# Performance work log

Measured on AMD Instinct MI355X. Metric: run time of the kernel, lower is better.

Reference implementation:

```python
import jax, jax.numpy as jnp
import numpy as np

H = 512  # hidden_size


def setup_inputs() -> dict:
    key = jax.random.key(0)
    ks = jax.random.split(key, 8)
    B, L = 16, 2048
    query = jax.random.normal(ks[0], (B, 1, 2 * H), dtype=jnp.float32)
    keys = jax.random.normal(ks[1], (B, L, 2 * H), dtype=jnp.float32)
    coverage = jax.random.uniform(ks[2], (B, L, 1), dtype=jnp.float32)
    # alignment MLP: Linear(4H+1 -> 2H, bias) -> tanh -> Linear(2H -> 1, no bias) -> softmax(dim=1)
    s1 = 1.0 / np.sqrt(4 * H + 1)
    W1 = jax.random.uniform(ks[3], (4 * H + 1, 2 * H), jnp.float32, -s1, s1)
    b1 = jax.random.uniform(ks[4], (2 * H,), jnp.float32, -s1, s1)
    s2 = 1.0 / np.sqrt(2 * H)
    W2 = jax.random.uniform(ks[5], (2 * H, 1), jnp.float32, -s2, s2)
    # reduce: Linear(2H -> H, no bias)
    Wr = jax.random.uniform(ks[6], (2 * H, H), jnp.float32, -s2, s2)
    return {"query": query, "keys": keys, "coverage": coverage,
            "W1": W1, "b1": b1, "W2": W2, "Wr": Wr}


def reference(query, keys, coverage, W1, b1, W2, Wr):
    B, L, _ = keys.shape
    q = jnp.broadcast_to(query, (B, L, query.shape[-1]))          # (B,L,2H)
    feat = jnp.concatenate([q, keys, coverage], axis=-1)          # (B,L,4H+1)
    h = jnp.tanh(feat @ W1 + b1)                                  # (B,L,2H)
    scores = h @ W2                                               # (B,L,1)
    attention = jax.nn.softmax(scores, axis=1)                    # softmax over length
    reduced = keys @ Wr                                           # (B,L,H)
    context = jnp.einsum('blo,blh->boh', attention, reduced)      # (B,1,H)
    return context, attention
```

## Files before the change

kernel.cpp:

```cpp
#include <hip/hip_runtime.h>
#include <hip/hip_bf16.h>
#include <stdint.h>

typedef short bf16x8 __attribute__((ext_vector_type(8)));
typedef float f32x4 __attribute__((ext_vector_type(4)));
typedef unsigned int u32x2 __attribute__((ext_vector_type(2)));

__device__ __forceinline__ uint32_t pack2f(float lo, float hi) {
  union { __hip_bfloat162 h; uint32_t u; } c;
  c.h.x = __float2bfloat16(lo);
  c.h.y = __float2bfloat16(hi);
  return c.u;
}

__device__ __forceinline__ unsigned short f32_to_bf16(float f) {
  union { __hip_bfloat16 h; unsigned short u; } c;
  c.h = __float2bfloat16(f);
  return c.u;
}

__device__ __forceinline__ float bfbits_to_f32(uint32_t hi16) {
  union { uint32_t u; float f; } c;
  c.u = hi16 << 16;
  return c.f;
}

__device__ __forceinline__ float fast_tanh(float x) {
  float e = __builtin_amdgcn_exp2f(x * 2.8853900817779268f);
  return 1.0f - 2.0f * __builtin_amdgcn_rcpf(e + 1.0f);
}

#define GLD16(g, l)                                                                    \
  __builtin_amdgcn_global_load_lds((const __attribute__((address_space(1))) void*)(g), \
                                   (__attribute__((address_space(3))) void*)(l), 16, 0, 0)

#define MFMA16(a, b, c) __builtin_amdgcn_mfma_f32_16x16x32_bf16(a, b, c, 0, 0, 0)
#define SBAR0() __builtin_amdgcn_sched_barrier(0)

__global__ void prep_kernel(const float* __restrict__ keys, unsigned short* __restrict__ keysbf,
                            const float* __restrict__ W1, unsigned short* __restrict__ W1kt,
                            const float* __restrict__ query, const float* __restrict__ b1,
                            float* __restrict__ qterm) {
  __shared__ __align__(16) unsigned char smem[16896];
  const int bid = blockIdx.x;
  const int t = threadIdx.x;
  if (bid < 256) {
    float (*tt)[65] = (float(*)[65])smem;
    const int kb = (bid & 15) * 64;
    const int jb = (bid >> 4) * 64;
    const int c = t & 63;
    const int r = t >> 6;
#pragma unroll
    for (int i = 0; i < 16; ++i) {
      const int k = i * 4 + r;
      tt[k][c] = W1[(size_t)(1024 + kb + k) * 1024 + (jb + c)];
    }
    __syncthreads();
#pragma unroll
    for (int i = 0; i < 16; ++i) {
      const int j = i * 4 + r;
      W1kt[(size_t)(jb + j) * 1024 + (kb + c)] = f32_to_bf16(tt[c][j]);
    }
  } else if (bid < 512) {
    float (*part)[64] = (float(*)[64])smem;
    const int q = bid - 256;
    const int b = q >> 4;
    const int j = (q & 15) * 64 + (t & 63);
    const int kq = t >> 6;
    const float* qp = query + b * 1024 + kq * 256;
    const float* wp = W1 + (size_t)(kq * 256) * 1024 + j;
    float acc = 0.f;
#pragma unroll 8
    for (int k = 0; k < 256; ++k) acc += qp[k] * wp[(size_t)k * 1024];
    part[kq][t & 63] = acc;
    __syncthreads();
    if (t < 64) {
      const int jj = (q & 15) * 64 + t;
      qterm[b * 1024 + jj] = b1[jj] + part[0][t] + part[1][t] + part[2][t] + part[3][t];
    }
  } else {
    const size_t base = (size_t)(bid - 512) * 16384;
#pragma unroll
    for (int bt = 0; bt < 2; ++bt) {
      f32x4 v[8];
#pragma unroll
      for (int i = 0; i < 8; ++i)
        v[i] = *(const f32x4*)(keys + base + bt * 8192 + i * 1024 + t * 4);
#pragma unroll
      for (int i = 0; i < 8; ++i) {
        u32x2 p;
        p.x = pack2f(v[i].x, v[i].y);
        p.y = pack2f(v[i].z, v[i].w);
        *(u32x2*)(keysbf + base + bt * 8192 + i * 1024 + t * 4) = p;
      }
    }
  }
}


#define V16_STAGE(kt_, P)                                            \
  GLD16(gkA + (kt_) * 64 + 0 * 65536, (P) + 0 * 8192 + t16);         \
  GLD16(gwB + (kt_) * 64 + 0 * 65536, (P) + 32768 + 0 * 8192 + t16); \
  GLD16(gkA + (kt_) * 64 + 1 * 65536, (P) + 1 * 8192 + t16);         \
  GLD16(gwB + (kt_) * 64 + 1 * 65536, (P) + 32768 + 1 * 8192 + t16); \
  GLD16(gkA + (kt_) * 64 + 2 * 65536, (P) + 2 * 8192 + t16);         \
  GLD16(gwB + (kt_) * 64 + 2 * 65536, (P) + 32768 + 2 * 8192 + t16); \
  GLD16(gkA + (kt_) * 64 + 3 * 65536, (P) + 3 * 8192 + t16);         \
  GLD16(gwB + (kt_) * 64 + 3 * 65536, (P) + 32768 + 3 * 8192 + t16);

#define V16_COMPUTE(P)                                                           \
  _Pragma("unroll") for (int kk = 0; kk < 2; ++kk) {                             \
    bf16x8 af[8], bfv[4];                                                        \
    _Pragma("unroll") for (int mf = 0; mf < 8; ++mf)                             \
        af[mf] = *(const bf16x8*)((P) + ((abase + mf * 2048) ^ (kk * 64)));      \
    _Pragma("unroll") for (int nf = 0; nf < 4; ++nf)                             \
        bfv[nf] = *(const bf16x8*)((P) + ((bbase + nf * 2048) ^ (kk * 64)));     \
    __builtin_amdgcn_s_setprio(1);                                               \
    _Pragma("unroll") for (int nf = 0; nf < 4; ++nf)                             \
        _Pragma("unroll") for (int mf = 0; mf < 8; ++mf) acc[mf][nf] =           \
            MFMA16(af[mf], bfv[nf], acc[mf][nf]);                                \
    __builtin_amdgcn_s_setprio(0);                                               \
  }

#define V16_ITER(t_, Pc, Ps, LAST)                            \
  asm volatile("s_waitcnt vmcnt(0) lgkmcnt(0)" ::: "memory"); \
  __builtin_amdgcn_s_barrier();                               \
  SBAR0();                                                    \
  if (!(LAST)) { V16_STAGE((t_) + 1, Ps); }                   \
  SBAR0();                                                    \
  V16_COMPUTE(Pc);

#define V16_PAIR(t0, t1)      \
  V16_ITER(t0, P0, P1, false) \
  V16_ITER(t1, P1, P0, (t1) == 15)

__global__ __launch_bounds__(512, 2) void gemm_score_v16(
    const unsigned short* __restrict__ keysbf, const unsigned short* __restrict__ W1kt,
    const float* __restrict__ qterm, const float* __restrict__ coverage,
    const float* __restrict__ W1, const float* __restrict__ W2,
    float* __restrict__ scores_part) {
  __shared__ __align__(16) unsigned char lds[135168];
  unsigned char* P0 = lds;
  unsigned char* P1 = lds + 65536;
  float* Sred = (float*)(lds + 131072);

  const int tid = threadIdx.x;
  const int bid = blockIdx.x;
  const int xcd = bid & 7;
  const int idx = bid >> 3;
  const int rowt = xcd * 16 + (idx >> 2);
  const int colgrp = idx & 3;
  const int row0 = rowt * 256;
  const int col0 = colgrp * 256;
  const int b = row0 >> 11;
  const int w = tid >> 6;
  const int wm = w >> 2, wn = w & 3;
  const int lane = tid & 63;
  const int c16 = lane & 15, q4 = lane >> 4;

  const int swzc = (q4 ^ (c16 & 7)) << 4;
  const int abase = (wm * 128 + c16) * 128 + swzc;
  const int bbase = 32768 + (wn * 64 + c16) * 128 + swzc;

  const int sr = tid >> 3;
  const int su = (tid & 7) ^ (sr & 7);
  const unsigned short* gkA = keysbf + (size_t)(row0 + sr) * 1024 + su * 8;
  const unsigned short* gwB = W1kt + (size_t)(col0 + sr) * 1024 + su * 8;
  const int t16 = tid * 16;

  f32x4 acc[8][4];
  const f32x4 zz = {0.f, 0.f, 0.f, 0.f};
#pragma unroll
  for (int mf = 0; mf < 8; ++mf)
#pragma unroll
    for (int nf = 0; nf < 4; ++nf) acc[mf][nf] = zz;

  V16_STAGE(0, P0);

  V16_PAIR(0, 1)
  V16_PAIR(2, 3)
  V16_PAIR(4, 5)
  V16_PAIR(6, 7)
  V16_PAIR(8, 9)
  V16_PAIR(10, 11)
  V16_PAIR(12, 13)
  V16_PAIR(14, 15)

  float covv[8][4];
#pragma unroll
  for (int mf = 0; mf < 8; ++mf)
#pragma unroll
    for (int r = 0; r < 4; ++r)
      covv[mf][r] = coverage[row0 + wm * 128 + mf * 16 + q4 * 4 + r];

  float p_part[8][4];
#pragma unroll
  for (int mf = 0; mf < 8; ++mf)
#pragma unroll
    for (int r = 0; r < 4; ++r) p_part[mf][r] = 0.f;

#pragma unroll
  for (int nf = 0; nf < 4; ++nf) {
    const int col = col0 + wn * 64 + nf * 16 + c16;
    const float qt = qterm[b * 1024 + col];
    const float w1c = W1[(size_t)2048 * 1024 + col];
    const float w2 = W2[col];
#pragma unroll
    for (int mf = 0; mf < 8; ++mf)
#pragma unroll
      for (int r = 0; r < 4; ++r) {
        float v = acc[mf][nf][r] + qt + covv[mf][r] * w1c;
        p_part[mf][r] += fast_tanh(v) * w2;
      }
  }

#pragma unroll
  for (int mf = 0; mf < 8; ++mf)
#pragma unroll
    for (int r = 0; r < 4; ++r) {
      float p = p_part[mf][r];
      p += __shfl_xor(p, 1);
      p += __shfl_xor(p, 2);
      p += __shfl_xor(p, 4);
      p += __shfl_xor(p, 8);
      if (c16 == 0) Sred[w * 128 + mf * 16 + q4 * 4 + r] = p;
    }
  __syncthreads();
  if (tid < 256) {
    const int wmv = tid >> 7, rl = tid & 127;
    float s = Sred[(wmv * 4 + 0) * 128 + rl] + Sred[(wmv * 4 + 1) * 128 + rl] +
              Sred[(wmv * 4 + 2) * 128 + rl] + Sred[(wmv * 4 + 3) * 128 + rl];
    scores_part[(size_t)colgrp * 32768 + row0 + tid] = s;
  }
}

__global__ void ctxpre_fused(const unsigned short* __restrict__ keysbf,
                             const float* __restrict__ sp, float* __restrict__ att,
                             float* __restrict__ ctx_part) {
  __shared__ float sc[2048];
  __shared__ float red[4];
  __shared__ float att_s[128];
  const int b = blockIdx.x;
  const int sl = blockIdx.y;
  const int tid = threadIdx.x;
  float mx = -1e30f;
  for (int l = tid; l < 2048; l += 256) {
    float v = 0.f;
#pragma unroll
    for (int g = 0; g < 4; ++g) v += sp[(size_t)g * 32768 + b * 2048 + l];
    sc[l] = v;
    mx = fmaxf(mx, v);
  }
#pragma unroll
  for (int o = 1; o < 64; o <<= 1) mx = fmaxf(mx, __shfl_xor(mx, o));
  if ((tid & 63) == 0) red[tid >> 6] = mx;
  __syncthreads();
  mx = fmaxf(fmaxf(red[0], red[1]), fmaxf(red[2], red[3]));
  __syncthreads();
  float sum = 0.f;
  for (int l = tid; l < 2048; l += 256) sum += __expf(sc[l] - mx);
#pragma unroll
  for (int o = 1; o < 64; o <<= 1) sum += __shfl_xor(sum, o);
  if ((tid & 63) == 0) red[tid >> 6] = sum;
  __syncthreads();
  const float inv = 1.0f / (red[0] + red[1] + red[2] + red[3]);
  if (tid < 128) {
    const float a = __expf(sc[sl * 128 + tid] - mx) * inv;
    att_s[tid] = a;
    att[b * 2048 + sl * 128 + tid] = a;
  }
  __syncthreads();

  const unsigned short* kb = keysbf + ((size_t)b * 2048 + sl * 128) * 1024 + tid * 4;
  f32x4 acc = {0.f, 0.f, 0.f, 0.f};
#pragma unroll 4
  for (int l = 0; l < 128; ++l) {
    u32x2 v = *(const u32x2*)(kb + (size_t)l * 1024);
    const float al = att_s[l];
    acc.x += bfbits_to_f32(v.x & 0xFFFFu) * al;
    acc.y += bfbits_to_f32(v.x >> 16) * al;
    acc.z += bfbits_to_f32(v.y & 0xFFFFu) * al;
    acc.w += bfbits_to_f32(v.y >> 16) * al;
  }
  *(f32x4*)(ctx_part + ((size_t)(sl * 16 + b)) * 1024 + tid * 4) = acc;
}

__global__ void ctx2_kernel(const float* __restrict__ ctx_part, const float* __restrict__ Wr,
                            float* __restrict__ out) {
  __shared__ float cpre[1024];
  __shared__ float part[4][64];
  const int hb = blockIdx.x;
  const int b = blockIdx.y;
  const int t = threadIdx.x;
#pragma unroll
  for (int jj = 0; jj < 4; ++jj) {
    const int j = jj * 256 + t;
    float s = 0.f;
#pragma unroll
    for (int sl = 0; sl < 16; ++sl) s += ctx_part[((size_t)(sl * 16 + b)) * 1024 + j];
    cpre[j] = s;
  }
  __syncthreads();
  const int h = hb * 64 + (t & 63);
  const int jq = t >> 6;
  const float* wp = Wr + (size_t)(jq * 256) * 512 + h;
  float acc = 0.f;
#pragma unroll 8
  for (int k = 0; k < 256; ++k) acc += cpre[jq * 256 + k] * wp[(size_t)k * 512];
  part[jq][t & 63] = acc;
  __syncthreads();
  if (t < 64)
    out[b * 512 + hb * 64 + t] = part[0][t] + part[1][t] + part[2][t] + part[3][t];
}

extern "C" void kernel_launch(void* const* d_in, const int* in_sizes, int n_in, void* d_out,
                              int out_size, void* d_ws, size_t ws_size, hipStream_t stream) {
  const float* query = (const float*)d_in[0];
  const float* keys = (const float*)d_in[1];
  const float* coverage = (const float*)d_in[2];
  const float* W1 = (const float*)d_in[3];
  const float* b1 = (const float*)d_in[4];
  const float* W2 = (const float*)d_in[5];
  const float* Wr = (const float*)d_in[6];
  float* out = (float*)d_out;
  char* ws = (char*)d_ws;

  float* scores_part = (float*)ws;
  float* ctx_part = (float*)(ws + 524288);
  float* qterm = (float*)(ws + 1638400);
  unsigned short* W1kt = (unsigned short*)(ws + 1703936);
  unsigned short* keysbf = (unsigned short*)(ws + 3801088);

  float* context_out = out;
  float* att_out = out + 8192;

  prep_kernel<<<dim3(2560), dim3(256), 0, stream>>>(keys, keysbf, W1, W1kt, query, b1, qterm);
  gemm_score_v16<<<dim3(512), dim3(512), 0, stream>>>(keysbf, W1kt, qterm, coverage, W1, W2,
                                                      scores_part);
  ctxpre_fused<<<dim3(16, 16), dim3(256), 0, stream>>>(keysbf, scores_part, att_out, ctx_part);
  ctx2_kernel<<<dim3(8, 16), dim3(256), 0, stream>>>(ctx_part, Wr, context_out);
}
```

Measured before the change: 131.4 us.

## Fuse keys fp32-to-bf16 conversion into GEMM A-operand load path

Removes the keys conversion blocks from the prep kernel. The GEMM now loads fp32 keys directly into registers, converts them to bf16, and writes them into swizzled LDS, prefetching two tiles ahead and waiting only on partial vmcnt. Blocks in column group 0 also write the bf16 keys to global memory for the later context kernel. This avoids a separate full pass over keys, but each of the four column groups re-reads fp32 keys, the staging goes through registers, and launch bounds drop to one block per CU.

```diff
diff --git a/kernel.cpp b/kernel.cpp
--- a/kernel.cpp
+++ b/kernel.cpp
@@ -37,10 +37,9 @@
 #define MFMA16(a, b, c) __builtin_amdgcn_mfma_f32_16x16x32_bf16(a, b, c, 0, 0, 0)
 #define SBAR0() __builtin_amdgcn_sched_barrier(0)
 
-__global__ void prep_kernel(const float* __restrict__ keys, unsigned short* __restrict__ keysbf,
-                            const float* __restrict__ W1, unsigned short* __restrict__ W1kt,
-                            const float* __restrict__ query, const float* __restrict__ b1,
-                            float* __restrict__ qterm) {
+__global__ void prep2_kernel(const float* __restrict__ W1, unsigned short* __restrict__ W1kt,
+                             const float* __restrict__ query, const float* __restrict__ b1,
+                             float* __restrict__ qterm) {
   __shared__ __align__(16) unsigned char smem[16896];
   const int bid = blockIdx.x;
   const int t = threadIdx.x;
@@ -61,7 +60,7 @@
       const int j = i * 4 + r;
       W1kt[(size_t)(jb + j) * 1024 + (kb + c)] = f32_to_bf16(tt[c][j]);
     }
-  } else if (bid < 512) {
+  } else {
     float (*part)[64] = (float(*)[64])smem;
     const int q = bid - 256;
     const int b = q >> 4;
@@ -78,37 +77,35 @@
       const int jj = (q & 15) * 64 + t;
       qterm[b * 1024 + jj] = b1[jj] + part[0][t] + part[1][t] + part[2][t] + part[3][t];
     }
-  } else {
-    const size_t base = (size_t)(bid - 512) * 16384;
-#pragma unroll
-    for (int bt = 0; bt < 2; ++bt) {
-      f32x4 v[8];
-#pragma unroll
-      for (int i = 0; i < 8; ++i)
-        v[i] = *(const f32x4*)(keys + base + bt * 8192 + i * 1024 + t * 4);
-#pragma unroll
-      for (int i = 0; i < 8; ++i) {
-        u32x2 p;
-        p.x = pack2f(v[i].x, v[i].y);
-        p.y = pack2f(v[i].z, v[i].w);
-        *(u32x2*)(keysbf + base + bt * 8192 + i * 1024 + t * 4) = p;
-      }
-    }
-  }
-}
-
-
-#define V16_STAGE(kt_, P)                                            \
-  GLD16(gkA + (kt_) * 64 + 0 * 65536, (P) + 0 * 8192 + t16);         \
+  }
+}
+
+
+#define V17_LOAD_A(kt_)                                \
+  _Pragma("unroll") for (int i = 0; i < 8; ++i)        \
+      Ar[i] = *(const f32x4*)(gkeys + (size_t)i * 32768 + (kt_) * 64);
+
+#define V17_PACK()                                     \
+  _Pragma("unroll") for (int i = 0; i < 8; ++i) {      \
+    pk[i].x = pack2f(Ar[i].x, Ar[i].y);                \
+    pk[i].y = pack2f(Ar[i].z, Ar[i].w);                \
+  }
+
+#define V17_WRITE_A(Ps)                                \
+  _Pragma("unroll") for (int i = 0; i < 8; ++i)        \
+      *(u32x2*)((Ps) + awof + i * 4096) = pk[i];
+
+#define V17_STORE(kt_)                                 \
+  _Pragma("unroll") for (int i = 0; i < 8; ++i)        \
+      *(u32x2*)(gkbf + (size_t)i * 32768 + (kt_) * 64) = pk[i];
+
+#define V17_STAGE_B(kt_, P)                                          \
   GLD16(gwB + (kt_) * 64 + 0 * 65536, (P) + 32768 + 0 * 8192 + t16); \
-  GLD16(gkA + (kt_) * 64 + 1 * 65536, (P) + 1 * 8192 + t16);         \
   GLD16(gwB + (kt_) * 64 + 1 * 65536, (P) + 32768 + 1 * 8192 + t16); \
-  GLD16(gkA + (kt_) * 64 + 2 * 65536, (P) + 2 * 8192 + t16);         \
   GLD16(gwB + (kt_) * 64 + 2 * 65536, (P) + 32768 + 2 * 8192 + t16); \
-  GLD16(gkA + (kt_) * 64 + 3 * 65536, (P) + 3 * 8192 + t16);         \
   GLD16(gwB + (kt_) * 64 + 3 * 65536, (P) + 32768 + 3 * 8192 + t16);
 
-#define V16_COMPUTE(P)                                                           \
+#define V17_COMPUTE(P)                                                           \
   _Pragma("unroll") for (int kk = 0; kk < 2; ++kk) {                             \
     bf16x8 af[8], bfv[4];                                                        \
     _Pragma("unroll") for (int mf = 0; mf < 8; ++mf)                             \
@@ -122,23 +119,32 @@
     __builtin_amdgcn_s_setprio(0);                                               \
   }
 
-#define V16_ITER(t_, Pc, Ps, LAST)                            \
-  asm volatile("s_waitcnt vmcnt(0) lgkmcnt(0)" ::: "memory"); \
-  __builtin_amdgcn_s_barrier();                               \
-  SBAR0();                                                    \
-  if (!(LAST)) { V16_STAGE((t_) + 1, Ps); }                   \
-  SBAR0();                                                    \
-  V16_COMPUTE(Pc);
-
-#define V16_PAIR(t0, t1)      \
-  V16_ITER(t0, P0, P1, false) \
-  V16_ITER(t1, P1, P0, (t1) == 15)
-
-__global__ __launch_bounds__(512, 2) void gemm_score_v16(
-    const unsigned short* __restrict__ keysbf, const unsigned short* __restrict__ W1kt,
-    const float* __restrict__ qterm, const float* __restrict__ coverage,
-    const float* __restrict__ W1, const float* __restrict__ W2,
-    float* __restrict__ scores_part) {
+#define V17_ITER(t_, Pc, Ps, LAST)                                       \
+  if (LAST) { asm volatile("s_waitcnt vmcnt(0) lgkmcnt(0)" ::: "memory"); } \
+  else      { asm volatile("s_waitcnt vmcnt(8) lgkmcnt(0)" ::: "memory"); } \
+  __builtin_amdgcn_s_barrier();                                          \
+  SBAR0();                                                               \
+  if (!(LAST)) {                                                         \
+    V17_PACK();                                                          \
+    V17_WRITE_A(Ps);                                                     \
+    if (cg0) { V17_STORE((t_) + 1); }                                    \
+    SBAR0();                                                             \
+    V17_STAGE_B((t_) + 1, Ps);                                           \
+    SBAR0();                                                             \
+    if ((t_) < 14) { V17_LOAD_A((t_) + 2); }                             \
+    SBAR0();                                                             \
+  }                                                                      \
+  V17_COMPUTE(Pc);
+
+#define V17_PAIR(t0, t1)      \
+  V17_ITER(t0, P0, P1, false) \
+  V17_ITER(t1, P1, P0, (t1) == 15)
+
+__global__ __launch_bounds__(512, 1) void gemm_score_v17(
+    const float* __restrict__ keys, unsigned short* __restrict__ keysbf,
+    const unsigned short* __restrict__ W1kt, const float* __restrict__ qterm,
+    const float* __restrict__ coverage, const float* __restrict__ W1,
+    const float* __restrict__ W2, float* __restrict__ scores_part) {
   __shared__ __align__(16) unsigned char lds[135168];
   unsigned char* P0 = lds;
   unsigned char* P1 = lds + 65536;
@@ -150,6 +156,7 @@
   const int idx = bid >> 3;
   const int rowt = xcd * 16 + (idx >> 2);
   const int colgrp = idx & 3;
+  const bool cg0 = (colgrp == 0);
   const int row0 = rowt * 256;
   const int col0 = colgrp * 256;
   const int b = row0 >> 11;
@@ -162,12 +169,19 @@
   const int abase = (wm * 128 + c16) * 128 + swzc;
   const int bbase = 32768 + (wn * 64 + c16) * 128 + swzc;
 
+  const int ar0 = tid >> 4;
+  const int kun = tid & 15;
+  const float* gkeys = keys + (size_t)(row0 + ar0) * 1024 + kun * 4;
+  unsigned short* gkbf = keysbf + (size_t)(row0 + ar0) * 1024 + kun * 4;
+  const int awof = ar0 * 128 + ((((kun >> 1) ^ (ar0 & 7)) << 4) + (kun & 1) * 8);
+
   const int sr = tid >> 3;
   const int su = (tid & 7) ^ (sr & 7);
-  const unsigned short* gkA = keysbf + (size_t)(row0 + sr) * 1024 + su * 8;
   const unsigned short* gwB = W1kt + (size_t)(col0 + sr) * 1024 + su * 8;
   const int t16 = tid * 16;
 
+  f32x4 Ar[8];
+  u32x2 pk[8];
   f32x4 acc[8][4];
   const f32x4 zz = {0.f, 0.f, 0.f, 0.f};
 #pragma unroll
@@ -175,16 +189,24 @@
 #pragma unroll
     for (int nf = 0; nf < 4; ++nf) acc[mf][nf] = zz;
 
-  V16_STAGE(0, P0);
-
-  V16_PAIR(0, 1)
-  V16_PAIR(2, 3)
-  V16_PAIR(4, 5)
-  V16_PAIR(6, 7)
-  V16_PAIR(8, 9)
-  V16_PAIR(10, 11)
-  V16_PAIR(12, 13)
-  V16_PAIR(14, 15)
+  V17_LOAD_A(0);
+  V17_PACK();
+  V17_WRITE_A(P0);
+  if (cg0) { V17_STORE(0); }
+  SBAR0();
+  V17_STAGE_B(0, P0);
+  SBAR0();
+  V17_LOAD_A(1);
+  SBAR0();
+
+  V17_PAIR(0, 1)
+  V17_PAIR(2, 3)
+  V17_PAIR(4, 5)
+  V17_PAIR(6, 7)
+  V17_PAIR(8, 9)
+  V17_PAIR(10, 11)
+  V17_PAIR(12, 13)
+  V17_PAIR(14, 15)
 
   float covv[8][4];
 #pragma unroll
@@ -334,9 +356,9 @@
   float* context_out = out;
   float* att_out = out + 8192;
 
-  prep_kernel<<<dim3(2560), dim3(256), 0, stream>>>(keys, keysbf, W1, W1kt, query, b1, qterm);
-  gemm_score_v16<<<dim3(512), dim3(512), 0, stream>>>(keysbf, W1kt, qterm, coverage, W1, W2,
-                                                      scores_part);
+  prep2_kernel<<<dim3(512), dim3(256), 0, stream>>>(W1, W1kt, query, b1, qterm);
+  gemm_score_v17<<<dim3(512), dim3(512), 0, stream>>>(keys, keysbf, W1kt, qterm, coverage, W1,
+                                                      W2, scores_part);
   ctxpre_fused<<<dim3(16, 16), dim3(256), 0, stream>>>(keysbf, scores_part, att_out, ctx_part);
   ctx2_kernel<<<dim3(8, 16), dim3(256), 0, stream>>>(ctx_part, Wr, context_out);
 }
```

Result: slower. 141.8 us (+7.9%).
